# Kernel tuning notes

Hardware: AMD Instinct MI355X
Metric: run time of the kernel (lower is better)

Reference implementation:

```python
import jax, jax.numpy as jnp
import numpy as np

ALPHA = 0.5  # distance-decay base (self.alpha)

def setup_inputs() -> dict:
    key = jax.random.key(0)
    N, E, D_IN, D_OUT = 50000, 800000, 128, 128
    k1, k2, k3, k4, k5 = jax.random.split(key, 5)
    h = jax.random.normal(k1, (N, D_IN), dtype=jnp.float32)
    # first N edges are self-loops so every node has in/out degree >= 1
    src = jnp.concatenate([jnp.arange(N), jax.random.randint(k2, (E - N,), 0, N)]).astype(jnp.int32)
    dst = jnp.concatenate([jnp.arange(N), jax.random.randint(k3, (E - N,), 0, N)]).astype(jnp.int32)
    distance = jax.random.randint(k4, (E,), 0, 6).astype(jnp.int32)
    limit = float(np.sqrt(6.0 / (D_IN + D_OUT)))  # xavier_uniform
    weight = jax.random.uniform(k5, (D_IN, D_OUT), jnp.float32, -limit, limit)
    bias = jnp.zeros((D_OUT,), jnp.float32)
    return {"h": h, "src": src, "dst": dst, "distance": distance, "weight": weight, "bias": bias}

def reference(h, src, dst, distance, weight, bias):
    N = h.shape[0]
    ones = jnp.ones(src.shape[0], jnp.float32)
    out_deg = jax.ops.segment_sum(ones, src, num_segments=N)  # [N]
    in_deg = jax.ops.segment_sum(ones, dst, num_segments=N)   # [N]
    # source-side symmetric norm
    feat = h * (out_deg ** -0.5)[:, None]                     # [N, D]
    # per-edge message: gathered src feature * alpha^distance
    w = jnp.power(jnp.float32(ALPHA), distance.astype(jnp.float32))  # [E]
    msg = feat[src] * w[:, None]                              # [E, D]
    # mean over mailbox == segment-sum / in-degree
    agg = jax.ops.segment_sum(msg, dst, num_segments=N) / in_deg[:, None]  # [N, D]
    rst = agg @ weight                                        # [N, D_OUT]
    rst = rst * (in_deg ** -0.5)[:, None] + bias
    return rst
```

## Files before the change

### kernel.cpp

```cpp
#include <hip/hip_runtime.h>


constexpr int D = 128;
constexpr int HC = 32;
constexpr int PNODES = 32;
constexpr int PCAP = 768;
constexpr int CHUNK = 8192;
constexpr int NCAST = 384;

typedef __attribute__((ext_vector_type(8))) short bf16x8;
typedef __attribute__((ext_vector_type(4))) float f32x4;

__device__ __forceinline__ float bf16_to_f(unsigned int u16) {
    union { unsigned int u; float f; } c; c.u = u16 << 16; return c.f;
}
__device__ __forceinline__ unsigned int f_to_bf16(float f) {
    union { float f; unsigned int u; } c; c.f = f;
    unsigned int u = c.u;
    u += 0x7fffu + ((u >> 16) & 1u);
    return u >> 16;
}

__global__ __launch_bounds__(256) void k_combo(const int* __restrict__ src,
        const int* __restrict__ dst, const int* __restrict__ dist,
        int* __restrict__ gcur, unsigned int* __restrict__ gbuf,
        unsigned int* __restrict__ gdeg,
        const float4* __restrict__ h4, uint4* __restrict__ hs4,
        const float* __restrict__ W, unsigned short* __restrict__ Wt,
        int E, int N, int NW, int hchunk, int P, int nbA) {
    extern __shared__ int dyn[];
    int tid = threadIdx.x;
    int bi = blockIdx.x;

    if (bi >= nbA + HC) {
        if (bi == nbA + HC) {
            for (int i = tid; i < D * D; i += 256) {
                int k = i >> 7, n = i & 127;
                Wt[n * D + k] = (unsigned short)f_to_bf16(W[i]);
            }
            return;
        }
        int cb = bi - (nbA + HC + 1);
        int G = N * (D / 8);
        for (int i = cb * 256 + tid; i < G; i += NCAST * 256) {
            float4 a = h4[2 * i];
            float4 b = h4[2 * i + 1];
            uint4 o;
            o.x = f_to_bf16(a.x) | (f_to_bf16(a.y) << 16);
            o.y = f_to_bf16(a.z) | (f_to_bf16(a.w) << 16);
            o.z = f_to_bf16(b.x) | (f_to_bf16(b.y) << 16);
            o.w = f_to_bf16(b.z) | (f_to_bf16(b.w) << 16);
            hs4[i] = o;
        }
        return;
    }

    if (bi >= nbA) {
        unsigned int* bins = (unsigned int*)dyn;
        for (int i = tid; i < NW; i += 256) bins[i] = 0;
        __syncthreads();
        int c = bi - nbA;
        int e0 = c * hchunk, e1 = min(e0 + hchunk, E);
        for (int i = e0 + tid * 4; i < e1; i += 1024) {
            if (i + 3 < e1) {
                int4 k4 = *(const int4*)&src[i];
                atomicAdd(&bins[k4.x >> 1], 1u << ((k4.x & 1) * 16));
                atomicAdd(&bins[k4.y >> 1], 1u << ((k4.y & 1) * 16));
                atomicAdd(&bins[k4.z >> 1], 1u << ((k4.z & 1) * 16));
                atomicAdd(&bins[k4.w >> 1], 1u << ((k4.w & 1) * 16));
            } else {
                for (int e = i; e < e1; e++)
                    atomicAdd(&bins[src[e] >> 1], 1u << ((src[e] & 1) * 16));
            }
        }
        __syncthreads();
        for (int i = tid; i < NW; i += 256) {
            unsigned int v = bins[i];
            if (v) atomicAdd(&gdeg[i], v);
        }
        return;
    }

    unsigned int* sorted = (unsigned int*)dyn;
    int* gidx  = dyn + CHUNK;
    int* hist  = dyn + 2 * CHUNK;
    int* start = hist + P;
    int* lofs  = start + P;
    int* base_g = lofs + P;
    __shared__ int wsum[4];

    int lane = tid & 63, w = tid >> 6;
    int e0 = bi * CHUNK;
    int e1 = min(e0 + CHUNK, E);
    int ce = e1 - e0;

    for (int b = tid; b < P; b += 256) hist[b] = 0;
    __syncthreads();

    for (int i = e0 + tid * 4; i < e1; i += 1024) {
        if (i + 3 < e1) {
            int4 d4 = *(const int4*)&dst[i];
            atomicAdd(&hist[d4.x >> 5], 1);
            atomicAdd(&hist[d4.y >> 5], 1);
            atomicAdd(&hist[d4.z >> 5], 1);
            atomicAdd(&hist[d4.w >> 5], 1);
        } else {
            for (int e = i; e < e1; e++) atomicAdd(&hist[dst[e] >> 5], 1);
        }
    }
    __syncthreads();

    int loc[7];
    int s = 0;
    #pragma unroll
    for (int j = 0; j < 7; j++) {
        int b = tid * 7 + j;
        int v = (b < P) ? hist[b] : 0;
        loc[j] = s;
        s += v;
    }
    int x = s;
    #pragma unroll
    for (int off = 1; off < 64; off <<= 1) {
        int t = __shfl_up(x, off, 64);
        if (lane >= off) x += t;
    }
    if (lane == 63) wsum[w] = x;
    __syncthreads();
    int tbase = x - s;
    #pragma unroll
    for (int k = 0; k < 4; k++) if (k < w) tbase += wsum[k];
    #pragma unroll
    for (int j = 0; j < 7; j++) {
        int b = tid * 7 + j;
        if (b < P) {
            int st = tbase + loc[j];
            start[b] = st;
            lofs[b] = st;
            int cnt = hist[b];
            if (cnt) base_g[b] = atomicAdd(&gcur[b], cnt);
        }
    }
    __syncthreads();

    for (int i = e0 + tid * 4; i < e1; i += 1024) {
        if (i + 3 < e1) {
            int4 s4 = *(const int4*)&src[i];
            int4 d4 = *(const int4*)&dst[i];
            int4 q4 = *(const int4*)&dist[i];
            #pragma unroll
            for (int j = 0; j < 4; j++) {
                int sv = (&s4.x)[j], dv = (&d4.x)[j], qv = (&q4.x)[j];
                int p = dv >> 5;
                unsigned int wd = (unsigned)sv | ((unsigned)(dv & 31) << 16)
                                | ((unsigned)qv << 21);
                int pos = atomicAdd(&lofs[p], 1);
                sorted[pos] = wd;
                int rank = base_g[p] + (pos - start[p]);
                gidx[pos] = (rank < PCAP) ? p * PCAP + rank : -1;
            }
        } else {
            for (int e = i; e < e1; e++) {
                int sv = src[e], dv = dst[e], qv = dist[e];
                int p = dv >> 5;
                unsigned int wd = (unsigned)sv | ((unsigned)(dv & 31) << 16)
                                | ((unsigned)qv << 21);
                int pos = atomicAdd(&lofs[p], 1);
                sorted[pos] = wd;
                int rank = base_g[p] + (pos - start[p]);
                gidx[pos] = (rank < PCAP) ? p * PCAP + rank : -1;
            }
        }
    }
    __syncthreads();

    for (int i = tid; i < ce; i += 256) {
        int g = gidx[i];
        if (g >= 0) gbuf[g] = sorted[i];
    }
}

__global__ __launch_bounds__(256, 6) void k_pagg(const uint4* __restrict__ hs4,
        const unsigned int* __restrict__ gbuf, const int* __restrict__ gcur,
        const unsigned short* __restrict__ gdeg16,
        const unsigned short* __restrict__ Wt, const float* __restrict__ bias,
        float* __restrict__ out, int N) {
    __shared__ unsigned int elist[PCAP];
    __shared__ unsigned int slist[PCAP];
    __shared__ int h2[PNODES], st2[PNODES], lo2[PNODES];
    __shared__ unsigned short As[PNODES * 136];
    int p = blockIdx.x;
    int tid = threadIdx.x;
    int cnt = min(gcur[p], PCAP);
    const unsigned int* gp = gbuf + (size_t)p * PCAP;

    if (tid < PNODES) h2[tid] = 0;
    __syncthreads();
    for (int i = tid; i < cnt; i += 256) {
        unsigned int wd = gp[i];
        elist[i] = wd;
        atomicAdd(&h2[(wd >> 16) & 31], 1);
    }
    __syncthreads();
    if (tid < 64) {
        int v = (tid < PNODES) ? h2[tid] : 0;
        int x = v;
        #pragma unroll
        for (int off = 1; off < 32; off <<= 1) {
            int t = __shfl_up(x, off, 64);
            if ((tid & 63) >= off) x += t;
        }
        if (tid < PNODES) { st2[tid] = x - v; lo2[tid] = x - v; }
    }
    __syncthreads();
    for (int i = tid; i < cnt; i += 256) {
        unsigned int wd = elist[i];
        int pos = atomicAdd(&lo2[(wd >> 16) & 31], 1);
        slist[pos] = wd;
    }
    __syncthreads();

    int wv = tid >> 6, l64 = tid & 63;
    int lane16 = l64 & 15, sub = l64 >> 4;
    #pragma unroll
    for (int k = 0; k < 8; k++) {
        int dl = wv * 8 + k;
        int node = p * PNODES + dl;
        int deg = h2[dl], b = st2[dl];
        float acc[8] = {0.f, 0.f, 0.f, 0.f, 0.f, 0.f, 0.f, 0.f};
        for (int eo = 0; eo < deg; eo += 16) {
            uint4 hv[4];
            float cc[4];
            #pragma unroll
            for (int j = 0; j < 4; j++) {
                int off = eo + j * 4 + sub;
                bool valid = off < deg;
                unsigned int wd = slist[b + (valid ? off : 0)];
                int sv = wd & 0xffff;
                float os = rsqrtf((float)gdeg16[sv]);
                cc[j] = valid ? __uint_as_float((127u - ((wd >> 21) & 7u)) << 23) * os
                              : 0.f;
                hv[j] = hs4[(size_t)sv * 16 + lane16];
            }
            #pragma unroll
            for (int j = 0; j < 4; j++) {
                float c = cc[j];
                acc[0] += c * bf16_to_f(hv[j].x & 0xffffu);
                acc[1] += c * bf16_to_f(hv[j].x >> 16);
                acc[2] += c * bf16_to_f(hv[j].y & 0xffffu);
                acc[3] += c * bf16_to_f(hv[j].y >> 16);
                acc[4] += c * bf16_to_f(hv[j].z & 0xffffu);
                acc[5] += c * bf16_to_f(hv[j].z >> 16);
                acc[6] += c * bf16_to_f(hv[j].w & 0xffffu);
                acc[7] += c * bf16_to_f(hv[j].w >> 16);
            }
        }
        #pragma unroll
        for (int j = 0; j < 8; j++) {
            acc[j] += __shfl_xor(acc[j], 16, 64);
            acc[j] += __shfl_xor(acc[j], 32, 64);
        }
        if (sub == 0) {
            uint4 o = make_uint4(0u, 0u, 0u, 0u);
            if (node < N) {
                float fd = (float)deg;
                float sc = rsqrtf(fd) / fd;
                o.x = f_to_bf16(acc[0] * sc) | (f_to_bf16(acc[1] * sc) << 16);
                o.y = f_to_bf16(acc[2] * sc) | (f_to_bf16(acc[3] * sc) << 16);
                o.z = f_to_bf16(acc[4] * sc) | (f_to_bf16(acc[5] * sc) << 16);
                o.w = f_to_bf16(acc[6] * sc) | (f_to_bf16(acc[7] * sc) << 16);
            }
            *(uint4*)&As[dl * 136 + lane16 * 8] = o;
        }
    }
    __syncthreads();

    int m = l64 & 15, quad = l64 >> 4;
    int mt = wv & 1, ntb = (wv >> 1) * 4;
    f32x4 acc2[4];
    #pragma unroll
    for (int t = 0; t < 4; t++) acc2[t] = (f32x4){0.f, 0.f, 0.f, 0.f};
    #pragma unroll
    for (int s = 0; s < 4; s++) {
        bf16x8 a = *(const bf16x8*)&As[(mt * 16 + m) * 136 + quad * 8 + s * 32];
        #pragma unroll
        for (int t = 0; t < 4; t++) {
            int n = (ntb + t) * 16 + m;
            bf16x8 b = *(const bf16x8*)&Wt[n * D + quad * 8 + s * 32];
            acc2[t] = __builtin_amdgcn_mfma_f32_16x16x32_bf16(a, b, acc2[t], 0, 0, 0);
        }
    }
    int orow0 = p * PNODES + mt * 16 + quad * 4;
    #pragma unroll
    for (int t = 0; t < 4; t++) {
        int n = (ntb + t) * 16 + m;
        float bz = bias[n];
        #pragma unroll
        for (int r = 0; r < 4; r++) {
            int grow = orow0 + r;
            if (grow < N) out[(size_t)grow * D + n] = acc2[t][r] + bz;
        }
    }
}

extern "C" void kernel_launch(void* const* d_in, const int* in_sizes, int n_in,
                              void* d_out, int out_size, void* d_ws, size_t ws_size,
                              hipStream_t stream) {
    const float* h    = (const float*)d_in[0];
    const int*   src  = (const int*)d_in[1];
    const int*   dst  = (const int*)d_in[2];
    const int*   dist = (const int*)d_in[3];
    const float* W    = (const float*)d_in[4];
    const float* bias = (const float*)d_in[5];
    float* out = (float*)d_out;
    const int N = in_sizes[0] / D;
    const int E = in_sizes[1];

    const int NW = (N + 1) / 2;
    const int hchunk = (((E + HC - 1) / HC) + 3) & ~3;
    const int P = (N + PNODES - 1) / PNODES;
    const int nbA = (E + CHUNK - 1) / CHUNK;

    char* ws = (char*)d_ws;
    size_t p = 0;
    auto alloc = [&](size_t bytes) -> char* {
        char* r = ws + p;
        p = (p + bytes + 511) & ~(size_t)511;
        return r;
    };
    int* gcur = (int*)alloc((size_t)P * 4);
    unsigned int* gdeg = (unsigned int*)alloc((size_t)NW * 4);
    unsigned int* gbuf = (unsigned int*)alloc((size_t)P * PCAP * 4);
    unsigned short* hs = (unsigned short*)alloc((size_t)N * D * 2);
    unsigned short* Wt = (unsigned short*)alloc((size_t)D * D * 2);

    size_t dyn_part = ((size_t)2 * CHUNK + 4 * P) * 4;
    size_t dyn_hist = (size_t)NW * 4;
    size_t dyn_sz = dyn_part > dyn_hist ? dyn_part : dyn_hist;

    hipMemsetAsync(gcur, 0, (size_t)((char*)gdeg - (char*)gcur) + (size_t)NW * 4,
                   stream);
    k_combo<<<nbA + HC + 1 + NCAST, 256, dyn_sz, stream>>>(src, dst, dist,
            gcur, gbuf, gdeg, (const float4*)h, (uint4*)hs, W, Wt,
            E, N, NW, hchunk, P, nbA);
    k_pagg<<<P, 256, 0, stream>>>((const uint4*)hs, gbuf, gcur,
            (const unsigned short*)gdeg, Wt, bias, out, N);
}
```

Before: 161.3 us.

## Store gathered features as fp16 and prefetch two nodes' first edge batches together

```diff
diff --git a/kernel.cpp b/kernel.cpp
--- a/kernel.cpp
+++ b/kernel.cpp
@@ -10,6 +10,7 @@
 
 typedef __attribute__((ext_vector_type(8))) short bf16x8;
 typedef __attribute__((ext_vector_type(4))) float f32x4;
+typedef __attribute__((ext_vector_type(2))) _Float16 f16x2;
 
 __device__ __forceinline__ float bf16_to_f(unsigned int u16) {
     union { unsigned int u; float f; } c; c.u = u16 << 16; return c.f;
@@ -19,6 +20,10 @@
     unsigned int u = c.u;
     u += 0x7fffu + ((u >> 16) & 1u);
     return u >> 16;
+}
+__device__ __forceinline__ unsigned int pack_f16x2(float x, float y) {
+    f16x2 p; p.x = (_Float16)x; p.y = (_Float16)y;
+    union { f16x2 h; unsigned int u; } c; c.h = p; return c.u;
 }
 
 __global__ __launch_bounds__(256) void k_combo(const int* __restrict__ src,
@@ -46,10 +51,10 @@
             float4 a = h4[2 * i];
             float4 b = h4[2 * i + 1];
             uint4 o;
-            o.x = f_to_bf16(a.x) | (f_to_bf16(a.y) << 16);
-            o.y = f_to_bf16(a.z) | (f_to_bf16(a.w) << 16);
-            o.z = f_to_bf16(b.x) | (f_to_bf16(b.y) << 16);
-            o.w = f_to_bf16(b.z) | (f_to_bf16(b.w) << 16);
+            o.x = pack_f16x2(a.x, a.y);
+            o.y = pack_f16x2(a.z, a.w);
+            o.z = pack_f16x2(b.x, b.y);
+            o.w = pack_f16x2(b.z, b.w);
             hs4[i] = o;
         }
         return;
@@ -222,39 +227,33 @@
 
     int wv = tid >> 6, l64 = tid & 63;
     int lane16 = l64 & 15, sub = l64 >> 4;
-    #pragma unroll
-    for (int k = 0; k < 8; k++) {
-        int dl = wv * 8 + k;
-        int node = p * PNODES + dl;
-        int deg = h2[dl], b = st2[dl];
-        float acc[8] = {0.f, 0.f, 0.f, 0.f, 0.f, 0.f, 0.f, 0.f};
-        for (int eo = 0; eo < deg; eo += 16) {
-            uint4 hv[4];
-            float cc[4];
+
+    auto load_batch = [&](int b, int eo, int deg, uint4* hv, float* cc) {
+        #pragma unroll
+        for (int j = 0; j < 4; j++) {
+            int off = eo + j * 4 + sub;
+            bool valid = off < deg;
+            unsigned int wd = slist[valid ? b + off : 0];
+            unsigned int sv = wd & 0xffffu;
+            float os = rsqrtf((float)gdeg16[sv]);
+            cc[j] = valid ? __uint_as_float((127u - ((wd >> 21) & 7u)) << 23) * os
+                          : 0.f;
+            hv[j] = hs4[(sv << 4) + (unsigned)lane16];
+        }
+    };
+    auto comp_batch = [&](const uint4* hv, const float* cc, float* acc) {
+        #pragma unroll
+        for (int j = 0; j < 4; j++) {
+            float c = cc[j];
+            const f16x2* hp = (const f16x2*)&hv[j];
             #pragma unroll
-            for (int j = 0; j < 4; j++) {
-                int off = eo + j * 4 + sub;
-                bool valid = off < deg;
-                unsigned int wd = slist[b + (valid ? off : 0)];
-                int sv = wd & 0xffff;
-                float os = rsqrtf((float)gdeg16[sv]);
-                cc[j] = valid ? __uint_as_float((127u - ((wd >> 21) & 7u)) << 23) * os
-                              : 0.f;
-                hv[j] = hs4[(size_t)sv * 16 + lane16];
-            }
-            #pragma unroll
-            for (int j = 0; j < 4; j++) {
-                float c = cc[j];
-                acc[0] += c * bf16_to_f(hv[j].x & 0xffffu);
-                acc[1] += c * bf16_to_f(hv[j].x >> 16);
-                acc[2] += c * bf16_to_f(hv[j].y & 0xffffu);
-                acc[3] += c * bf16_to_f(hv[j].y >> 16);
-                acc[4] += c * bf16_to_f(hv[j].z & 0xffffu);
-                acc[5] += c * bf16_to_f(hv[j].z >> 16);
-                acc[6] += c * bf16_to_f(hv[j].w & 0xffffu);
-                acc[7] += c * bf16_to_f(hv[j].w >> 16);
-            }
-        }
+            for (int q = 0; q < 4; q++) {
+                acc[2 * q]     = fmaf((float)hp[q].x, c, acc[2 * q]);
+                acc[2 * q + 1] = fmaf((float)hp[q].y, c, acc[2 * q + 1]);
+            }
+        }
+    };
+    auto fold_store = [&](int dl, int deg, float* acc) {
         #pragma unroll
         for (int j = 0; j < 8; j++) {
             acc[j] += __shfl_xor(acc[j], 16, 64);
@@ -262,7 +261,7 @@
         }
         if (sub == 0) {
             uint4 o = make_uint4(0u, 0u, 0u, 0u);
-            if (node < N) {
+            if (p * PNODES + dl < N) {
                 float fd = (float)deg;
                 float sc = rsqrtf(fd) / fd;
                 o.x = f_to_bf16(acc[0] * sc) | (f_to_bf16(acc[1] * sc) << 16);
@@ -272,6 +271,31 @@
             }
             *(uint4*)&As[dl * 136 + lane16 * 8] = o;
         }
+    };
+
+    #pragma unroll
+    for (int kp = 0; kp < 4; kp++) {
+        int dlA = wv * 8 + kp * 2, dlB = dlA + 1;
+        int degA = h2[dlA], bA = st2[dlA];
+        int degB = h2[dlB], bB = st2[dlB];
+        uint4 hvA[4], hvB[4];
+        float ccA[4], ccB[4];
+        load_batch(bA, 0, degA, hvA, ccA);
+        load_batch(bB, 0, degB, hvB, ccB);
+        float accA[8] = {0.f, 0.f, 0.f, 0.f, 0.f, 0.f, 0.f, 0.f};
+        comp_batch(hvA, ccA, accA);
+        for (int eo = 16; eo < degA; eo += 16) {
+            load_batch(bA, eo, degA, hvA, ccA);
+            comp_batch(hvA, ccA, accA);
+        }
+        fold_store(dlA, degA, accA);
+        float accB[8] = {0.f, 0.f, 0.f, 0.f, 0.f, 0.f, 0.f, 0.f};
+        comp_batch(hvB, ccB, accB);
+        for (int eo = 16; eo < degB; eo += 16) {
+            load_batch(bB, eo, degB, hvB, ccB);
+            comp_batch(hvB, ccB, accB);
+        }
+        fold_store(dlB, degB, accB);
     }
     __syncthreads();
 
```

Result: no change. 162.3 us (+0.7%).
